# Optimization experiments

Hardware: AMD Instinct MI355X
Metric: run time of the kernel (lower is better)

## Reference

```python
import jax, jax.numpy as jnp
import numpy as np
import math

B, S, D, H, L = 2, 2048, 2048, 16, 512
HD = D // H          # head dim = 128
DIM_KV = 256         # scale = sqrt(DIM_KV // 2) = sqrt(128)
EPS = 1e-5


def _layer_norm(x, g, b):
    m = jnp.mean(x, axis=-1, keepdims=True)
    v = jnp.var(x, axis=-1, keepdims=True)
    return (x - m) * jax.lax.rsqrt(v + EPS) * g + b


def setup_inputs() -> dict:
    key = jax.random.key(0)
    ks = jax.random.split(key, 10)
    s = 0.02
    return {
        "x": jax.random.normal(ks[0], (B, S, D), dtype=jnp.float32),
        "mask": jnp.zeros((B, S), dtype=bool),  # True = padded position
        "wq_down": jax.random.normal(ks[1], (D, L), dtype=jnp.float32) * s,
        "bq_down": jnp.zeros((L,), dtype=jnp.float32),
        "gq_ln": jnp.ones((L,), dtype=jnp.float32),
        "bq_ln": jnp.zeros((L,), dtype=jnp.float32),
        "wq_up": jax.random.normal(ks[2], (L, D), dtype=jnp.float32) * s,
        "bq_up": jnp.zeros((D,), dtype=jnp.float32),
        "wkv_down": jax.random.normal(ks[3], (D, L), dtype=jnp.float32) * s,
        "bkv_down": jnp.zeros((L,), dtype=jnp.float32),
        "gkv_ln": jnp.ones((L,), dtype=jnp.float32),
        "bkv_ln": jnp.zeros((L,), dtype=jnp.float32),
        "wkv_up": jax.random.normal(ks[4], (L, 2 * D), dtype=jnp.float32) * s,
        "bkv_up": jnp.zeros((2 * D,), dtype=jnp.float32),
        "w_out": jax.random.normal(ks[5], (D, D), dtype=jnp.float32) * s,
        "b_out": jnp.zeros((D,), dtype=jnp.float32),
    }


def reference(x, mask, wq_down, bq_down, gq_ln, bq_ln, wq_up, bq_up,
              wkv_down, bkv_down, gkv_ln, bkv_ln, wkv_up, bkv_up, w_out, b_out):
    # low-rank query path: down-proj -> LN -> up-proj
    q_lat = _layer_norm(x @ wq_down + bq_down, gq_ln, bq_ln)      # [B,S,L]
    q = q_lat @ wq_up + bq_up                                      # [B,S,D]
    # low-rank KV path (compressed_kv is the MLA latent / cache entry)
    kv_lat = _layer_norm(x @ wkv_down + bkv_down, gkv_ln, bkv_ln)  # [B,S,L]
    kv = kv_lat @ wkv_up + bkv_up                                  # [B,S,2D]
    k, v = jnp.split(kv, 2, axis=-1)                               # [B,S,D] each

    def heads(t):
        return t.reshape(B, S, H, HD).transpose(0, 2, 1, 3)        # [B,H,S,HD]

    qh, kh, vh = heads(q), heads(k), heads(v)
    scale = 1.0 / math.sqrt(DIM_KV // 2)
    scores = jnp.einsum('bhqd,bhkd->bhqk', qh, kh) * scale          # [B,H,S,S]
    neg_inf = jnp.finfo(scores.dtype).min
    # padding mask (True = masked) broadcast over heads and queries
    scores = jnp.where(mask[:, None, None, :], neg_inf, scores)
    causal = jnp.triu(jnp.ones((S, S), dtype=bool), k=1)
    scores = jnp.where(causal, neg_inf, scores)
    attn = jax.nn.softmax(scores, axis=-1)
    out = jnp.einsum('bhqk,bhkd->bhqd', attn, vh)                   # [B,H,S,HD]
    out = out.transpose(0, 2, 1, 3).reshape(B, S, D)
    return out @ w_out + b_out
```

## Files before the change

### kernel.cpp

```cpp
#include <hip/hip_runtime.h>
#include <math.h>
#include <type_traits>

typedef unsigned short u16;
typedef __attribute__((ext_vector_type(8))) short bf16x8;
typedef __attribute__((ext_vector_type(4))) float f32x4;

#define B_  2
#define S_  2048
#define D_  2048
#define H_  16
#define HD_ 128
#define L_  512
constexpr float EPS   = 1e-5f;
constexpr float SCALE = 0.08838834764831845f;

__device__ __forceinline__ u16 f2bf(float x) {
    unsigned u = __float_as_uint(x);
    u += 0x7fffu + ((u >> 16) & 1u);
    return (u16)(u >> 16);
}
__device__ __forceinline__ float bf2f(u16 v) {
    return __uint_as_float(((unsigned)v) << 16);
}

__device__ __forceinline__ void gl_lds16(const u16* g, u16* l) {
    __builtin_amdgcn_global_load_lds(
        (const __attribute__((address_space(1))) unsigned int*)g,
        (__attribute__((address_space(3))) unsigned int*)l, 16, 0, 0);
}

template <typename OutT, int BN>
__global__ __launch_bounds__(256)
void gemm_mfma_kernel(const u16* __restrict__ A, const u16* __restrict__ Bt,
                      const float* __restrict__ biasA,
                      const float* __restrict__ biasB, OutT* __restrict__ C,
                      int M, int N, int K, int lda, int ldc, int nsplit) {
    constexpr int NJ = BN / 32;
    __shared__ __align__(16) u16 As[128 * 32];
    __shared__ __align__(16) u16 Bs[BN * 32];

    const int tid  = threadIdx.x;
    const int wave = tid >> 6, lane = tid & 63;
    const int l15  = lane & 15, g = lane >> 4;
    const int wm   = wave >> 1, wn = wave & 1;
    const int m0   = blockIdx.y * 128, n0 = blockIdx.x * BN;

    const int sr = lane >> 2;
    const int sc = lane & 3;
    const int swz = (l15 >> 1) & 3;

    f32x4 acc[4][NJ];
#pragma unroll
    for (int i = 0; i < 4; ++i)
#pragma unroll
        for (int j = 0; j < NJ; ++j) acc[i][j] = (f32x4)0.f;

    for (int k0 = 0; k0 < K; k0 += 32) {
#pragma unroll
        for (int t = 0; t < 2; ++t) {
            const int r  = wave * 32 + t * 16 + sr;
            const int c  = sc ^ ((r >> 1) & 3);
            gl_lds16(A + (size_t)(m0 + r) * lda + k0 + c * 8,
                     &As[(wave * 32 + t * 16) * 32]);
        }
#pragma unroll
        for (int t = 0; t < BN / 64; ++t) {
            const int r  = wave * (BN / 4) + t * 16 + sr;
            const int c  = sc ^ ((r >> 1) & 3);
            gl_lds16(Bt + (size_t)(n0 + r) * K + k0 + c * 8,
                     &Bs[(wave * (BN / 4) + t * 16) * 32]);
        }
        __syncthreads();

        bf16x8 af[4], bfr[NJ];
#pragma unroll
        for (int i = 0; i < 4; ++i) {
            const int ra = wm * 64 + i * 16 + l15;
            af[i]  = *(const bf16x8*)&As[ra * 32 + (g ^ swz) * 8];
        }
#pragma unroll
        for (int j = 0; j < NJ; ++j) {
            const int rb = wn * (BN / 2) + j * 16 + l15;
            bfr[j] = *(const bf16x8*)&Bs[rb * 32 + (g ^ swz) * 8];
        }
#pragma unroll
        for (int i = 0; i < 4; ++i)
#pragma unroll
            for (int j = 0; j < NJ; ++j)
                acc[i][j] = __builtin_amdgcn_mfma_f32_16x16x32_bf16(
                    af[i], bfr[j], acc[i][j], 0, 0, 0);
        __syncthreads();
    }

#pragma unroll
    for (int j = 0; j < NJ; ++j) {
        const int n  = n0 + wn * (BN / 2) + j * 16 + l15;
        const float bv = (n < nsplit) ? biasA[n] : biasB[n - nsplit];
#pragma unroll
        for (int i = 0; i < 4; ++i) {
            const int mb = m0 + wm * 64 + i * 16 + g * 4;
#pragma unroll
            for (int r = 0; r < 4; ++r) {
                float v = acc[i][j][r] + bv;
                if constexpr (std::is_same_v<OutT, float>)
                    C[(size_t)(mb + r) * ldc + n] = v;
                else
                    C[(size_t)(mb + r) * ldc + n] = f2bf(v);
            }
        }
    }
}

__global__ __launch_bounds__(256)
void up_gemm_kernel(const u16* __restrict__ lat,
                    const u16* __restrict__ wkvu_t, const u16* __restrict__ wqu_t,
                    const float* __restrict__ bkv_up, const float* __restrict__ bq_up,
                    u16* __restrict__ k_bf, u16* __restrict__ vt,
                    u16* __restrict__ q_bf) {
    __shared__ __align__(16) u16 As[128 * 32];
    __shared__ __align__(16) u16 Bs[128 * 32];

    const int bx    = blockIdx.x;
    const bool iskv = bx < 32;
    const u16* A    = iskv ? lat + L_ : lat;
    const u16* Bt   = iskv ? wkvu_t : wqu_t;
    const float* bias = iskv ? bkv_up : bq_up;
    const int n0    = (iskv ? bx : bx - 32) * 128;
    const int m0    = blockIdx.y * 128;
    constexpr int K = L_, lda = 2 * L_;

    const int tid  = threadIdx.x;
    const int wave = tid >> 6, lane = tid & 63;
    const int l15  = lane & 15, g = lane >> 4;
    const int wm   = wave >> 1, wn = wave & 1;

    const int sr = lane >> 2;
    const int sc = lane & 3;
    const int swz = (l15 >> 1) & 3;

    f32x4 acc[4][4];
#pragma unroll
    for (int i = 0; i < 4; ++i)
#pragma unroll
        for (int j = 0; j < 4; ++j) acc[i][j] = (f32x4)0.f;

    for (int k0 = 0; k0 < K; k0 += 32) {
#pragma unroll
        for (int t = 0; t < 2; ++t) {
            const int r  = wave * 32 + t * 16 + sr;
            const int c  = sc ^ ((r >> 1) & 3);
            gl_lds16(A  + (size_t)(m0 + r) * lda + k0 + c * 8,
                     &As[(wave * 32 + t * 16) * 32]);
            gl_lds16(Bt + (size_t)(n0 + r) * K + k0 + c * 8,
                     &Bs[(wave * 32 + t * 16) * 32]);
        }
        __syncthreads();

        bf16x8 af[4], bfr[4];
#pragma unroll
        for (int i = 0; i < 4; ++i) {
            const int ra = wm * 64 + i * 16 + l15;
            af[i]  = *(const bf16x8*)&As[ra * 32 + (g ^ swz) * 8];
            const int rb = wn * 64 + i * 16 + l15;
            bfr[i] = *(const bf16x8*)&Bs[rb * 32 + (g ^ swz) * 8];
        }
#pragma unroll
        for (int i = 0; i < 4; ++i)
#pragma unroll
            for (int j = 0; j < 4; ++j)
                acc[i][j] = __builtin_amdgcn_mfma_f32_16x16x32_bf16(
                    af[i], bfr[j], acc[i][j], 0, 0, 0);
        __syncthreads();
    }

    const bool vstore = iskv && (n0 >= D_);
#pragma unroll
    for (int j = 0; j < 4; ++j) {
        const int n  = n0 + wn * 64 + j * 16 + l15;
        const float bv = bias[n];
        if (vstore) {
            const int dg = n - D_;
            const int hh = dg >> 7, dd = dg & 127;
            u16* vrow = vt + ((size_t)(((m0 >> 11) * H_ + hh) * HD_ + dd)) * S_;
#pragma unroll
            for (int i = 0; i < 4; ++i) {
                const int mb = m0 + wm * 64 + i * 16 + g * 4;
                ushort4 o;
                o.x = f2bf(acc[i][j][0] + bv);
                o.y = f2bf(acc[i][j][1] + bv);
                o.z = f2bf(acc[i][j][2] + bv);
                o.w = f2bf(acc[i][j][3] + bv);
                *(ushort4*)&vrow[mb & (S_ - 1)] = o;
            }
        } else {
            u16* C = iskv ? k_bf : q_bf;
#pragma unroll
            for (int i = 0; i < 4; ++i) {
                const int mb = m0 + wm * 64 + i * 16 + g * 4;
#pragma unroll
                for (int r = 0; r < 4; ++r)
                    C[(size_t)(mb + r) * D_ + n] = f2bf(acc[i][j][r] + bv);
            }
        }
    }
}

__global__ __launch_bounds__(256)
void prep_kernel(const float* __restrict__ wqd,  const float* __restrict__ wkvd,
                 const float* __restrict__ wqu,  const float* __restrict__ wkvu,
                 const float* __restrict__ wo,   const float* __restrict__ x,
                 u16* __restrict__ wd_t,  u16* __restrict__ wqu_t,
                 u16* __restrict__ wkvu_t, u16* __restrict__ wout_t,
                 u16* __restrict__ x_bf) {
    int bid = blockIdx.x;
    if (bid >= 2304) {
        const int i = (bid - 2304) * 256 + threadIdx.x;
        float4 f = ((const float4*)x)[i];
        ushort4 o;
        o.x = f2bf(f.x); o.y = f2bf(f.y); o.z = f2bf(f.z); o.w = f2bf(f.w);
        ((ushort4*)x_bf)[i] = o;
        return;
    }
    const float* W; u16* Wt; int K, N;
    if (bid < 256)       { W = wqd;  Wt = wd_t;                      K = 2048; N = 512; }
    else if (bid < 512)  { W = wkvd; Wt = wd_t + (size_t)512 * 2048; K = 2048; N = 512;  bid -= 256; }
    else if (bid < 768)  { W = wqu;  Wt = wqu_t;                     K = 512;  N = 2048; bid -= 512; }
    else if (bid < 1280) { W = wkvu; Wt = wkvu_t;                    K = 512;  N = 4096; bid -= 768; }
    else                 { W = wo;   Wt = wout_t;                    K = 2048; N = 2048; bid -= 1280; }
    const int nblk = N / 64;
    const int n0 = (bid % nblk) * 64, k0 = (bid / nblk) * 64;

    __shared__ u16 T[64][72];
    const int t = threadIdx.x;
    {
        const int kr = t >> 2, nc = (t & 3) * 16;
#pragma unroll
        for (int v = 0; v < 4; ++v) {
            float4 f = *(const float4*)&W[(size_t)(k0 + kr) * N + n0 + nc + v * 4];
            T[nc + v * 4 + 0][kr] = f2bf(f.x);
            T[nc + v * 4 + 1][kr] = f2bf(f.y);
            T[nc + v * 4 + 2][kr] = f2bf(f.z);
            T[nc + v * 4 + 3][kr] = f2bf(f.w);
        }
    }
    __syncthreads();
    {
        const int nr = t >> 2, kc = (t & 3) * 16;
        union { u16 u[16]; uint4 q[2]; } o;
#pragma unroll
        for (int i = 0; i < 16; ++i) o.u[i] = T[nr][kc + i];
        uint4* dst = (uint4*)&Wt[(size_t)(n0 + nr) * K + k0 + kc];
        dst[0] = o.q[0]; dst[1] = o.q[1];
    }
}

__global__ __launch_bounds__(256)
void layernorm_fused_kernel(u16* __restrict__ buf,
                            const float* __restrict__ gq,
                            const float* __restrict__ bq,
                            const float* __restrict__ gkv,
                            const float* __restrict__ bkv) {
    const int r    = blockIdx.x;
    const int half = r & 1;
    u16* p = buf + (size_t)(r >> 1) * 1024 + half * 512;
    const float* g    = half ? gkv : gq;
    const float* bvec = half ? bkv : bq;
    const int tid = threadIdx.x;

    float x0 = bf2f(p[tid]), x1 = bf2f(p[tid + 256]);
    float s  = x0 + x1;
    float sq = x0 * x0 + x1 * x1;

    __shared__ float red[8];
    __shared__ float stats[2];

#pragma unroll
    for (int off = 32; off; off >>= 1) {
        s  += __shfl_down(s, off);
        sq += __shfl_down(sq, off);
    }
    const int wave = tid >> 6;
    if ((tid & 63) == 0) { red[wave] = s; red[wave + 4] = sq; }
    __syncthreads();
    if (tid == 0) {
        float ts = red[0] + red[1] + red[2] + red[3];
        float tq = red[4] + red[5] + red[6] + red[7];
        float mean = ts / (float)L_;
        float var  = tq / (float)L_ - mean * mean;
        stats[0] = mean;
        stats[1] = rsqrtf(var + EPS);
    }
    __syncthreads();
    const float mean = stats[0], rstd = stats[1];
    p[tid]       = f2bf((x0 - mean) * rstd * g[tid]       + bvec[tid]);
    p[tid + 256] = f2bf((x1 - mean) * rstd * g[tid + 256] + bvec[tid + 256]);
}

#define PPITCH 72

__global__ __launch_bounds__(256)
void flash_attn_kernel(const u16* __restrict__ qbf, const u16* __restrict__ kbf,
                       const u16* __restrict__ vt,
                       const unsigned char* __restrict__ mask,
                       u16* __restrict__ out) {
    const int x    = blockIdx.x;
    const int qgrp = (S_ / 64 - 1) - (x >> 5);
    const int hb   = x & 31;
    const int h    = hb >> 1, b = hb & 1;
    const int tid  = threadIdx.x;
    const int wave = tid >> 6, lane = tid & 63;
    const int l15  = lane & 15, g = lane >> 4;
    const int q0   = qgrp * 64 + wave * 16;

    __shared__ __align__(16) u16 Ks[2][64][128];
    __shared__ __align__(16) u16 Vs[2][128][64];
    __shared__ __align__(16) u16 Pl[4][16][PPITCH];

    const u16* kbase = kbf + (size_t)b * S_ * D_ + h * HD_;
    const u16* vbase = vt + (size_t)((b * H_ + h) * HD_) * S_;
    const unsigned char* mbase = mask + b * S_;

    const int kr_l = lane >> 4;
    const int kb_l = (lane & 15) * 16;
    const int vr_l = lane >> 3;
    const int vb_l = (lane & 7) * 16;

    auto STAGE = [&](int bi, int k0s) {
#pragma unroll
        for (int j = 0; j < 4; ++j) {
            const int rr = wave * 16 + j * 4 + kr_l;
            gl_lds16(kbase + (size_t)(k0s + rr) * D_ +
                         ((kb_l ^ ((rr & 7) << 4)) >> 1),
                     &Ks[bi][wave * 16 + j * 4][0]);
            const int rv = wave * 32 + j * 8 + vr_l;
            gl_lds16(vbase + (size_t)rv * S_ + k0s +
                         ((vb_l ^ ((rv & 7) << 4)) >> 1),
                     &Vs[bi][wave * 32 + j * 8][0]);
        }
    };

    bf16x8 qf[4];
#pragma unroll
    for (int c = 0; c < 4; ++c)
        qf[c] = *(const bf16x8*)(qbf +
            (size_t)(b * S_ + q0 + l15) * D_ + h * HD_ + c * 32 + g * 8);

    bf16x8 ones;
#pragma unroll
    for (int j = 0; j < 8; ++j) ones[j] = (short)0x3f80;

    f32x4 o[8];
#pragma unroll
    for (int i = 0; i < 8; ++i) o[i] = (f32x4)0.f;
    f32x4 osum = (f32x4)0.f;

    const int qb  = q0 + 4 * g;
    const int ksw = (l15 & 7) << 4;
    const int nt  = qgrp + 1;

    STAGE(0, 0);
    __syncthreads();

    for (int kt = 0; kt < nt; ++kt) {
        const int k0  = kt * 64;
        const int cur = kt & 1;
        if (kt + 1 < nt) STAGE(cur ^ 1, k0 + 64);

        float nb[4];
#pragma unroll
        for (int cc = 0; cc < 4; ++cc)
            nb[cc] = mbase[k0 + cc * 16 + l15] ? -INFINITY : -8.0f;

        f32x4 s[4];
#pragma unroll
        for (int cc = 0; cc < 4; ++cc) {
            bf16x8 kf[4];
#pragma unroll
            for (int c = 0; c < 4; ++c)
                kf[c] = *(const bf16x8*)&Ks[cur][cc * 16 + l15]
                    [((c * 64 + g * 16) ^ ksw) >> 1];
            f32x4 t = (f32x4)0.f;
#pragma unroll
            for (int c = 0; c < 4; ++c)
                t = __builtin_amdgcn_mfma_f32_16x16x32_bf16(qf[c], kf[c], t, 0, 0, 0);
            s[cc] = t;
        }

#pragma unroll
        for (int cc = 0; cc < 4; ++cc)
#pragma unroll
            for (int r = 0; r < 4; ++r)
                s[cc][r] = fmaf(s[cc][r], SCALE, nb[cc]);

        if (kt == nt - 1) {
#pragma unroll
            for (int cc = 0; cc < 4; ++cc) {
                const int kk = k0 + cc * 16 + l15;
#pragma unroll
                for (int r = 0; r < 4; ++r)
                    if (kk > qb + r) s[cc][r] = -INFINITY;
            }
        }

#pragma unroll
        for (int cc = 0; cc < 4; ++cc)
#pragma unroll
            for (int r = 0; r < 4; ++r)
                Pl[wave][4 * g + r][cc * 16 + l15] = f2bf(__expf(s[cc][r]));

        const bf16x8 pf0 = *(const bf16x8*)&Pl[wave][l15][g * 8];
        const bf16x8 pf1 = *(const bf16x8*)&Pl[wave][l15][32 + g * 8];

#pragma unroll
        for (int i = 0; i < 8; ++i) {
            bf16x8 vf0 = *(const bf16x8*)&Vs[cur][16 * i + l15]
                [((g * 16) ^ ksw) >> 1];
            bf16x8 vf1 = *(const bf16x8*)&Vs[cur][16 * i + l15]
                [((g * 16 + 64) ^ ksw) >> 1];
            o[i] = __builtin_amdgcn_mfma_f32_16x16x32_bf16(pf0, vf0, o[i], 0, 0, 0);
            o[i] = __builtin_amdgcn_mfma_f32_16x16x32_bf16(pf1, vf1, o[i], 0, 0, 0);
        }
        osum = __builtin_amdgcn_mfma_f32_16x16x32_bf16(pf0, ones, osum, 0, 0, 0);
        osum = __builtin_amdgcn_mfma_f32_16x16x32_bf16(pf1, ones, osum, 0, 0, 0);

        __syncthreads();
    }

    float inv[4];
#pragma unroll
    for (int r = 0; r < 4; ++r) inv[r] = 1.0f / osum[r];
#pragma unroll
    for (int i = 0; i < 8; ++i)
#pragma unroll
        for (int r = 0; r < 4; ++r)
            out[(size_t)(b * S_ + q0 + 4 * g + r) * D_ +
                h * HD_ + 16 * i + l15] = f2bf(o[i][r] * inv[r]);
}

extern "C" void kernel_launch(void* const* d_in, const int* in_sizes, int n_in,
                              void* d_out, int out_size, void* d_ws, size_t ws_size,
                              hipStream_t stream) {
    const float* x        = (const float*)d_in[0];
    const unsigned char* mask = (const unsigned char*)d_in[1];
    const float* wq_down  = (const float*)d_in[2];
    const float* bq_down  = (const float*)d_in[3];
    const float* gq_ln    = (const float*)d_in[4];
    const float* bq_ln    = (const float*)d_in[5];
    const float* wq_up    = (const float*)d_in[6];
    const float* bq_up    = (const float*)d_in[7];
    const float* wkv_down = (const float*)d_in[8];
    const float* bkv_down = (const float*)d_in[9];
    const float* gkv_ln   = (const float*)d_in[10];
    const float* bkv_ln   = (const float*)d_in[11];
    const float* wkv_up   = (const float*)d_in[12];
    const float* bkv_up   = (const float*)d_in[13];
    const float* w_out    = (const float*)d_in[14];
    const float* b_out    = (const float*)d_in[15];
    float* out = (float*)d_out;

    char* ws = (char*)d_ws;
    u16* x_bf    = (u16*)(ws);
    u16* vt      = (u16*)(ws);
    u16* lat     = (u16*)(ws + (16u << 20));
    u16* attn_bf = (u16*)(ws + (16u << 20));
    u16* wd_t    = (u16*)(ws + (24u << 20));
    u16* wkvu_t  = (u16*)(ws + (28u << 20));
    u16* wqu_t   = (u16*)(ws + (32u << 20));
    u16* wout_t  = (u16*)(ws + (34u << 20));
    u16* q_bf    = (u16*)(ws + (42u << 20));
    u16* k_bf    = (u16*)(ws + (58u << 20));

    const int M = B_ * S_;
    dim3 blk(256);

    prep_kernel<<<10496, blk, 0, stream>>>(
        wq_down, wkv_down, wq_up, wkv_up, w_out, x,
        wd_t, wqu_t, wkvu_t, wout_t, x_bf);

    gemm_mfma_kernel<u16, 64><<<dim3((2 * L_) / 64, M / 128), blk, 0, stream>>>(
        x_bf, wd_t, bq_down, bkv_down, lat,
        M, 2 * L_, D_, D_, 2 * L_, L_);

    layernorm_fused_kernel<<<2 * M, blk, 0, stream>>>(lat, gq_ln, bq_ln, gkv_ln, bkv_ln);

    up_gemm_kernel<<<dim3(48, M / 128), blk, 0, stream>>>(
        lat, wkvu_t, wqu_t, bkv_up, bq_up, k_bf, vt, q_bf);

    flash_attn_kernel<<<dim3((S_ / 64) * H_ * B_), blk, 0, stream>>>(
        q_bf, k_bf, vt, mask, attn_bf);

    gemm_mfma_kernel<float, 128><<<dim3(D_ / 128, M / 128), blk, 0, stream>>>(
        attn_bf, wout_t, b_out, b_out, out,
        M, D_, D_, D_, D_, D_);
}
```

Baseline: 336.6 us.

## Single-buffer V tile, split PV into halves, and use exp2 with folded log2e

The V tile in flash attention drops from double to single buffering and is loaded at the start of each iteration. A barrier before the PV stage makes sure the load has landed. The P staging buffer is halved by writing and consuming P in two 32-key halves, each followed by its PV MFMAs. The score scale and shift now fold in log2(e), so the kernel can use exp2f. Together these cut LDS per block, which should allow more resident blocks per CU, but V loads now overlap only with the QK^T compute and each iteration gains an extra barrier.

Measured after the change: 338.3 us. About the same (+0.5%).

```diff
diff --git a/kernel.cpp b/kernel.cpp
--- a/kernel.cpp
+++ b/kernel.cpp
@@ -14,6 +14,8 @@
 #define L_  512
 constexpr float EPS   = 1e-5f;
 constexpr float SCALE = 0.08838834764831845f;
+constexpr float SCALE_L2E = 0.12751701840172524f;
+constexpr float SHIFT2    = -11.541560327111707f;
 
 __device__ __forceinline__ u16 f2bf(float x) {
     unsigned u = __float_as_uint(x);
@@ -297,7 +299,7 @@
     p[tid + 256] = f2bf((x1 - mean) * rstd * g[tid + 256] + bvec[tid + 256]);
 }
 
-#define PPITCH 72
+#define PPITCH 40
 
 __global__ __launch_bounds__(256)
 void flash_attn_kernel(const u16* __restrict__ qbf, const u16* __restrict__ kbf,
@@ -314,7 +316,7 @@
     const int q0   = qgrp * 64 + wave * 16;
 
     __shared__ __align__(16) u16 Ks[2][64][128];
-    __shared__ __align__(16) u16 Vs[2][128][64];
+    __shared__ __align__(16) u16 Vs[128][64];
     __shared__ __align__(16) u16 Pl[4][16][PPITCH];
 
     const u16* kbase = kbf + (size_t)b * S_ * D_ + h * HD_;
@@ -326,17 +328,22 @@
     const int vr_l = lane >> 3;
     const int vb_l = (lane & 7) * 16;
 
-    auto STAGE = [&](int bi, int k0s) {
+    auto STAGE_K = [&](int bi, int k0s) {
 #pragma unroll
         for (int j = 0; j < 4; ++j) {
             const int rr = wave * 16 + j * 4 + kr_l;
             gl_lds16(kbase + (size_t)(k0s + rr) * D_ +
                          ((kb_l ^ ((rr & 7) << 4)) >> 1),
                      &Ks[bi][wave * 16 + j * 4][0]);
+        }
+    };
+    auto STAGE_V = [&](int k0s) {
+#pragma unroll
+        for (int j = 0; j < 4; ++j) {
             const int rv = wave * 32 + j * 8 + vr_l;
             gl_lds16(vbase + (size_t)rv * S_ + k0s +
                          ((vb_l ^ ((rv & 7) << 4)) >> 1),
-                     &Vs[bi][wave * 32 + j * 8][0]);
+                     &Vs[wave * 32 + j * 8][0]);
         }
     };
 
@@ -359,18 +366,19 @@
     const int ksw = (l15 & 7) << 4;
     const int nt  = qgrp + 1;
 
-    STAGE(0, 0);
+    STAGE_K(0, 0);
     __syncthreads();
 
     for (int kt = 0; kt < nt; ++kt) {
         const int k0  = kt * 64;
         const int cur = kt & 1;
-        if (kt + 1 < nt) STAGE(cur ^ 1, k0 + 64);
+        STAGE_V(k0);
+        if (kt + 1 < nt) STAGE_K(cur ^ 1, k0 + 64);
 
         float nb[4];
 #pragma unroll
         for (int cc = 0; cc < 4; ++cc)
-            nb[cc] = mbase[k0 + cc * 16 + l15] ? -INFINITY : -8.0f;
+            nb[cc] = mbase[k0 + cc * 16 + l15] ? -INFINITY : SHIFT2;
 
         f32x4 s[4];
 #pragma unroll
@@ -391,7 +399,7 @@
         for (int cc = 0; cc < 4; ++cc)
 #pragma unroll
             for (int r = 0; r < 4; ++r)
-                s[cc][r] = fmaf(s[cc][r], SCALE, nb[cc]);
+                s[cc][r] = fmaf(s[cc][r], SCALE_L2E, nb[cc]);
 
         if (kt == nt - 1) {
 #pragma unroll
@@ -403,25 +411,32 @@
             }
         }
 
-#pragma unroll
-        for (int cc = 0; cc < 4; ++cc)
+        __syncthreads();
+
+#pragma unroll
+        for (int cc = 0; cc < 2; ++cc)
 #pragma unroll
             for (int r = 0; r < 4; ++r)
-                Pl[wave][4 * g + r][cc * 16 + l15] = f2bf(__expf(s[cc][r]));
-
+                Pl[wave][4 * g + r][cc * 16 + l15] = f2bf(exp2f(s[cc][r]));
         const bf16x8 pf0 = *(const bf16x8*)&Pl[wave][l15][g * 8];
-        const bf16x8 pf1 = *(const bf16x8*)&Pl[wave][l15][32 + g * 8];
-
 #pragma unroll
         for (int i = 0; i < 8; ++i) {
-            bf16x8 vf0 = *(const bf16x8*)&Vs[cur][16 * i + l15]
-                [((g * 16) ^ ksw) >> 1];
-            bf16x8 vf1 = *(const bf16x8*)&Vs[cur][16 * i + l15]
-                [((g * 16 + 64) ^ ksw) >> 1];
-            o[i] = __builtin_amdgcn_mfma_f32_16x16x32_bf16(pf0, vf0, o[i], 0, 0, 0);
-            o[i] = __builtin_amdgcn_mfma_f32_16x16x32_bf16(pf1, vf1, o[i], 0, 0, 0);
+            bf16x8 vf = *(const bf16x8*)&Vs[16 * i + l15][((g * 16) ^ ksw) >> 1];
+            o[i] = __builtin_amdgcn_mfma_f32_16x16x32_bf16(pf0, vf, o[i], 0, 0, 0);
         }
         osum = __builtin_amdgcn_mfma_f32_16x16x32_bf16(pf0, ones, osum, 0, 0, 0);
+
+#pragma unroll
+        for (int cc = 2; cc < 4; ++cc)
+#pragma unroll
+            for (int r = 0; r < 4; ++r)
+                Pl[wave][4 * g + r][(cc - 2) * 16 + l15] = f2bf(exp2f(s[cc][r]));
+        const bf16x8 pf1 = *(const bf16x8*)&Pl[wave][l15][g * 8];
+#pragma unroll
+        for (int i = 0; i < 8; ++i) {
+            bf16x8 vf = *(const bf16x8*)&Vs[16 * i + l15][((g * 16 + 64) ^ ksw) >> 1];
+            o[i] = __builtin_amdgcn_mfma_f32_16x16x32_bf16(pf1, vf, o[i], 0, 0, 0);
+        }
         osum = __builtin_amdgcn_mfma_f32_16x16x32_bf16(pf1, ones, osum, 0, 0, 0);
 
         __syncthreads();
```
